# Kernel tuning notes

Measured on AMD Instinct MI355X. Metric: run time of the kernel, lower is better.

The kernel has to match this reference:

```python
import jax, jax.numpy as jnp
import numpy as np

B = 2          # batch size (fixed constant; torch code derives it from coords[:,0].max()+1)
C = 64         # NUM_BEV_FEATURES
NX = NY = 480  # grid_size, nz == 1
NXC = NYC = 960  # hardcoded 'cen' grid


def _make_coords(key, P, b, ny, nx):
    kb, ky, kx = jax.random.split(key, 3)
    bi = jax.random.randint(kb, (P,), 0, b, dtype=jnp.int32)
    z = jnp.zeros((P,), jnp.int32)
    y = jax.random.randint(ky, (P,), 0, ny, dtype=jnp.int32)
    x = jax.random.randint(kx, (P,), 0, nx, dtype=jnp.int32)
    return jnp.stack([bi, z, y, x], axis=1)


def setup_inputs() -> dict:
    key = jax.random.key(0)
    ks = jax.random.split(key, 8)
    return {
        "radar_cen_pillar_features": jax.random.normal(ks[0], (8000, C), jnp.float32),
        "radar_cen_coords": _make_coords(ks[1], 8000, B, NYC, NXC),
        "lidar_cen_pillar_features": jax.random.normal(ks[2], (30000, C), jnp.float32),
        "lidar_cen_coords": _make_coords(ks[3], 30000, B, NYC, NXC),
        "lidar_pillar_features": jax.random.normal(ks[4], (30000, C), jnp.float32),
        "lidar_coords": _make_coords(ks[5], 30000, B, NY, NX),
        "radar_pillar_features": jax.random.normal(ks[6], (8000, C), jnp.float32),
        "radar_coords": _make_coords(ks[7], 8000, B, NY, NX),
    }


def _scatter_bev(feat, coords, ny, nx):
    # feat [P, C], coords [P, 4] = (b, z, y, x); flat index = z + y*nx + x (nz==1 so z==0)
    idx = coords[:, 1] + coords[:, 2] * nx + coords[:, 3]
    grid = jnp.zeros((B, ny * nx, feat.shape[1]), feat.dtype)
    grid = grid.at[coords[:, 0], idx].set(feat)
    # -> [B, C, ny, nx]
    return grid.transpose(0, 2, 1).reshape(B, feat.shape[1], ny, nx)


def _maxpool2(x):
    # AdaptiveMaxPool2d(480) on 960x960 == 2x2 max pool
    b, c, h, w = x.shape
    return x.reshape(b, c, h // 2, 2, w // 2, 2).max(axis=(3, 5))


def reference(radar_cen_pillar_features, radar_cen_coords,
              lidar_cen_pillar_features, lidar_cen_coords,
              lidar_pillar_features, lidar_coords,
              radar_pillar_features, radar_coords):
    radar_cen = _maxpool2(_scatter_bev(radar_cen_pillar_features, radar_cen_coords, NYC, NXC))
    lidar_cen = _maxpool2(_scatter_bev(lidar_cen_pillar_features, lidar_cen_coords, NYC, NXC))
    lidar = _scatter_bev(lidar_pillar_features, lidar_coords, NY, NX)
    radar = _scatter_bev(radar_pillar_features, radar_coords, NY, NX)
    cat = jnp.concatenate(
        [jnp.concatenate([lidar, lidar_cen], axis=1),
         jnp.concatenate([radar, radar_cen], axis=1)], axis=1)
    return lidar, radar, cat
```

## Files before the change

kernel.cpp:

```cpp
#include <hip/hip_runtime.h>

#define NX   480
#define NXC  960
#define NS   (480*480)
#define NSC  (960*960)
#define CC   64
#define BB   2

__global__ void scatter_winner(const int* __restrict__ coords, int P, int nx, int ns,
                               int* __restrict__ winner ) {
    int p = blockIdx.x * blockDim.x + threadIdx.x;
    if (p >= P) return;
    int b = coords[4*p + 0];
    int y = coords[4*p + 2];
    int x = coords[4*p + 3];
    atomicMax(&winner[b*ns + y*nx + x], p);
}

__device__ __forceinline__ float term(int w, const float* __restrict__ f, int c) {
    return (w < 0) ? 0.0f : f[(size_t)w * CC + c];
}

__global__ void __launch_bounds__(256)
dense_write(const float* __restrict__ lf,  const float* __restrict__ rf,
            const float* __restrict__ lcf, const float* __restrict__ rcf,
            const int* __restrict__ wl,  const int* __restrict__ wr,
            const int* __restrict__ wlc, const int* __restrict__ wrc,
            float* __restrict__ out_l, float* __restrict__ out_r,
            float* __restrict__ out_cat) {
    int s = (blockIdx.x * 256 + threadIdx.x) * 4;
    int b = blockIdx.y;
    int c0 = blockIdx.z * 16;

    int4 v_l = *(const int4*)(wl + (size_t)b*NS + s);
    int4 v_r = *(const int4*)(wr + (size_t)b*NS + s);
    int wla[4] = {v_l.x, v_l.y, v_l.z, v_l.w};
    int wra[4] = {v_r.x, v_r.y, v_r.z, v_r.w};

    int py = s / NX, px = s - py * NX;
    int y0 = py * 2, x0 = px * 2;
    const int* blc = wlc + (size_t)b * NSC;
    const int* brc = wrc + (size_t)b * NSC;
    int4 lt0 = *(const int4*)(blc + (size_t)y0*NXC + x0);
    int4 lt1 = *(const int4*)(blc + (size_t)y0*NXC + x0 + 4);
    int4 lb0 = *(const int4*)(blc + (size_t)(y0+1)*NXC + x0);
    int4 lb1 = *(const int4*)(blc + (size_t)(y0+1)*NXC + x0 + 4);
    int4 rt0 = *(const int4*)(brc + (size_t)y0*NXC + x0);
    int4 rt1 = *(const int4*)(brc + (size_t)y0*NXC + x0 + 4);
    int4 rb0 = *(const int4*)(brc + (size_t)(y0+1)*NXC + x0);
    int4 rb1 = *(const int4*)(brc + (size_t)(y0+1)*NXC + x0 + 4);
    int lct[8] = {lt0.x, lt0.y, lt0.z, lt0.w, lt1.x, lt1.y, lt1.z, lt1.w};
    int lcb[8] = {lb0.x, lb0.y, lb0.z, lb0.w, lb1.x, lb1.y, lb1.z, lb1.w};
    int rct[8] = {rt0.x, rt0.y, rt0.z, rt0.w, rt1.x, rt1.y, rt1.z, rt1.w};
    int rcb[8] = {rb0.x, rb0.y, rb0.z, rb0.w, rb1.x, rb1.y, rb1.z, rb1.w};

    size_t so  = (size_t)b * CC  * NS + s;
    size_t co  = (size_t)b * 256 * NS + s;

    for (int cc = 0; cc < 16; ++cc) {
        int c = c0 + cc;
        float vl[4], vr[4], vlc[4], vrc[4];
        #pragma unroll
        for (int j = 0; j < 4; ++j) {
            vl[j] = term(wla[j], lf, c);
            vr[j] = term(wra[j], rf, c);
            float a = term(lct[2*j], lcf, c);
            a = fmaxf(a, term(lct[2*j+1], lcf, c));
            a = fmaxf(a, term(lcb[2*j],   lcf, c));
            a = fmaxf(a, term(lcb[2*j+1], lcf, c));
            vlc[j] = a;
            float m = term(rct[2*j], rcf, c);
            m = fmaxf(m, term(rct[2*j+1], rcf, c));
            m = fmaxf(m, term(rcb[2*j],   rcf, c));
            m = fmaxf(m, term(rcb[2*j+1], rcf, c));
            vrc[j] = m;
        }
        float4 fvl = make_float4(vl[0], vl[1], vl[2], vl[3]);
        float4 fvr = make_float4(vr[0], vr[1], vr[2], vr[3]);
        float4 fvlc = make_float4(vlc[0], vlc[1], vlc[2], vlc[3]);
        float4 fvrc = make_float4(vrc[0], vrc[1], vrc[2], vrc[3]);
        *(float4*)(out_l   + so + (size_t)c * NS)        = fvl;
        *(float4*)(out_r   + so + (size_t)c * NS)        = fvr;
        *(float4*)(out_cat + co + (size_t)c * NS)        = fvl;
        *(float4*)(out_cat + co + (size_t)(64  + c)*NS)  = fvlc;
        *(float4*)(out_cat + co + (size_t)(128 + c)*NS)  = fvr;
        *(float4*)(out_cat + co + (size_t)(192 + c)*NS)  = fvrc;
    }
}

extern "C" void kernel_launch(void* const* d_in, const int* in_sizes, int n_in,
                              void* d_out, int out_size, void* d_ws, size_t ws_size,
                              hipStream_t stream) {
    const float* rc_feat   = (const float*)d_in[0];
    const int*   rc_coords = (const int*)  d_in[1];
    const float* lc_feat   = (const float*)d_in[2];
    const int*   lc_coords = (const int*)  d_in[3];
    const float* l_feat    = (const float*)d_in[4];
    const int*   l_coords  = (const int*)  d_in[5];
    const float* r_feat    = (const float*)d_in[6];
    const int*   r_coords  = (const int*)  d_in[7];

    int P_rc = in_sizes[0] / CC;
    int P_lc = in_sizes[2] / CC;
    int P_l  = in_sizes[4] / CC;
    int P_r  = in_sizes[6] / CC;

    float* out_lidar = (float*)d_out;
    float* out_radar = out_lidar + (size_t)BB*CC*NS;
    float* out_cat   = out_radar + (size_t)BB*CC*NS;

    int* w_l  = (int*)d_ws;
    int* w_r  = w_l  + BB*NS;
    int* w_lc = w_r  + BB*NS;
    int* w_rc = w_lc + BB*NSC;
    size_t ws_bytes = (size_t)(2*BB*NS + 2*BB*NSC) * sizeof(int);

    hipMemsetAsync(d_ws, 0xFF, ws_bytes, stream);

    scatter_winner<<<(P_l  + 255)/256, 256, 0, stream>>>(l_coords,  P_l,  NX,  NS,  w_l);
    scatter_winner<<<(P_r  + 255)/256, 256, 0, stream>>>(r_coords,  P_r,  NX,  NS,  w_r);
    scatter_winner<<<(P_lc + 255)/256, 256, 0, stream>>>(lc_coords, P_lc, NXC, NSC, w_lc);
    scatter_winner<<<(P_rc + 255)/256, 256, 0, stream>>>(rc_coords, P_rc, NXC, NSC, w_rc);

    dim3 grid(NS / (256 * 4), BB, 4);
    dense_write<<<grid, 256, 0, stream>>>(l_feat, r_feat, lc_feat, rc_feat,
                                          w_l, w_r, w_lc, w_rc,
                                          out_lidar, out_radar, out_cat);
}
```

Before: 751.9 us.

## Fuse scatter launches, use nontemporal stores, and double channels per block

The four scatter_winner launches are merged into one kernel that picks its source descriptor from blockIdx.y, which cuts launch overhead. The dense write now uses nontemporal vector stores for the large output so it does not pollute the cache. Each block now handles 32 channels instead of 16, halving the grid z dimension so the winner-index loads are reused across more channels. The trade-off is fewer blocks in flight for the write-bound kernel.

```diff
diff --git a/kernel.cpp b/kernel.cpp
--- a/kernel.cpp
+++ b/kernel.cpp
@@ -7,14 +7,25 @@
 #define CC   64
 #define BB   2
 
-__global__ void scatter_winner(const int* __restrict__ coords, int P, int nx, int ns,
-                               int* __restrict__ winner ) {
-    int p = blockIdx.x * blockDim.x + threadIdx.x;
-    if (p >= P) return;
-    int b = coords[4*p + 0];
-    int y = coords[4*p + 2];
-    int x = coords[4*p + 3];
-    atomicMax(&winner[b*ns + y*nx + x], p);
+typedef float f4v __attribute__((ext_vector_type(4)));
+
+__device__ __forceinline__ void nt_store4(float* p, float a, float b, float c, float d) {
+    f4v v = {a, b, c, d};
+    __builtin_nontemporal_store(v, (f4v*)p);
+}
+
+struct SrcDesc { const int* coords; int* winner; int P; int nx; int ns; };
+
+__global__ void __launch_bounds__(256)
+scatter_winner4(SrcDesc s0, SrcDesc s1, SrcDesc s2, SrcDesc s3) {
+    SrcDesc d = (blockIdx.y == 0) ? s0 : (blockIdx.y == 1) ? s1
+              : (blockIdx.y == 2) ? s2 : s3;
+    int p = blockIdx.x * 256 + threadIdx.x;
+    if (p >= d.P) return;
+    int b = d.coords[4*p + 0];
+    int y = d.coords[4*p + 2];
+    int x = d.coords[4*p + 3];
+    atomicMax(&d.winner[b*d.ns + y*d.nx + x], p);
 }
 
 __device__ __forceinline__ float term(int w, const float* __restrict__ f, int c) {
@@ -30,7 +41,7 @@
             float* __restrict__ out_cat) {
     int s = (blockIdx.x * 256 + threadIdx.x) * 4;
     int b = blockIdx.y;
-    int c0 = blockIdx.z * 16;
+    int c0 = blockIdx.z * 32;
 
     int4 v_l = *(const int4*)(wl + (size_t)b*NS + s);
     int4 v_r = *(const int4*)(wr + (size_t)b*NS + s);
@@ -57,7 +68,7 @@
     size_t so  = (size_t)b * CC  * NS + s;
     size_t co  = (size_t)b * 256 * NS + s;
 
-    for (int cc = 0; cc < 16; ++cc) {
+    for (int cc = 0; cc < 32; ++cc) {
         int c = c0 + cc;
         float vl[4], vr[4], vlc[4], vrc[4];
         #pragma unroll
@@ -75,16 +86,12 @@
             m = fmaxf(m, term(rcb[2*j+1], rcf, c));
             vrc[j] = m;
         }
-        float4 fvl = make_float4(vl[0], vl[1], vl[2], vl[3]);
-        float4 fvr = make_float4(vr[0], vr[1], vr[2], vr[3]);
-        float4 fvlc = make_float4(vlc[0], vlc[1], vlc[2], vlc[3]);
-        float4 fvrc = make_float4(vrc[0], vrc[1], vrc[2], vrc[3]);
-        *(float4*)(out_l   + so + (size_t)c * NS)        = fvl;
-        *(float4*)(out_r   + so + (size_t)c * NS)        = fvr;
-        *(float4*)(out_cat + co + (size_t)c * NS)        = fvl;
-        *(float4*)(out_cat + co + (size_t)(64  + c)*NS)  = fvlc;
-        *(float4*)(out_cat + co + (size_t)(128 + c)*NS)  = fvr;
-        *(float4*)(out_cat + co + (size_t)(192 + c)*NS)  = fvrc;
+        nt_store4(out_l   + so + (size_t)c * NS,       vl[0],  vl[1],  vl[2],  vl[3]);
+        nt_store4(out_r   + so + (size_t)c * NS,       vr[0],  vr[1],  vr[2],  vr[3]);
+        nt_store4(out_cat + co + (size_t)c * NS,       vl[0],  vl[1],  vl[2],  vl[3]);
+        nt_store4(out_cat + co + (size_t)(64 +c)*NS,   vlc[0], vlc[1], vlc[2], vlc[3]);
+        nt_store4(out_cat + co + (size_t)(128+c)*NS,   vr[0],  vr[1],  vr[2],  vr[3]);
+        nt_store4(out_cat + co + (size_t)(192+c)*NS,   vrc[0], vrc[1], vrc[2], vrc[3]);
     }
 }
 
@@ -117,12 +124,15 @@
 
     hipMemsetAsync(d_ws, 0xFF, ws_bytes, stream);
 
-    scatter_winner<<<(P_l  + 255)/256, 256, 0, stream>>>(l_coords,  P_l,  NX,  NS,  w_l);
-    scatter_winner<<<(P_r  + 255)/256, 256, 0, stream>>>(r_coords,  P_r,  NX,  NS,  w_r);
-    scatter_winner<<<(P_lc + 255)/256, 256, 0, stream>>>(lc_coords, P_lc, NXC, NSC, w_lc);
-    scatter_winner<<<(P_rc + 255)/256, 256, 0, stream>>>(rc_coords, P_rc, NXC, NSC, w_rc);
+    SrcDesc s_l  = { l_coords,  w_l,  P_l,  NX,  NS  };
+    SrcDesc s_r  = { r_coords,  w_r,  P_r,  NX,  NS  };
+    SrcDesc s_lc = { lc_coords, w_lc, P_lc, NXC, NSC };
+    SrcDesc s_rc = { rc_coords, w_rc, P_rc, NXC, NSC };
+    int maxP = max(max(P_l, P_r), max(P_lc, P_rc));
+    dim3 wgrid((maxP + 255) / 256, 4);
+    scatter_winner4<<<wgrid, 256, 0, stream>>>(s_l, s_r, s_lc, s_rc);
 
-    dim3 grid(NS / (256 * 4), BB, 4);
+    dim3 grid(NS / (256 * 4), BB, 2);
     dense_write<<<grid, 256, 0, stream>>>(l_feat, r_feat, lc_feat, rc_feat,
                                           w_l, w_r, w_lc, w_rc,
                                           out_lidar, out_radar, out_cat);
```

Measured after the change: 739.6 us. Within noise of the previous version (-1.6%).
